# Performance work log

Hardware: AMD Instinct MI355X
Metric: run time of the kernel (lower is better)

## Reference

```python
import jax, jax.numpy as jnp
import numpy as np

N = 50000      # nodes
E = 800000     # edges (before self loops)
NFEAT = 128
HEADS = 4
NCLASS = 32    # per-head out channels of each GATConv
NHID = HEADS * NCLASS  # 128, inter-layer width
NEG_SLOPE = 0.2


def setup_inputs() -> dict:
    key = jax.random.key(0)
    ks = jax.random.split(key, 10)
    x = jax.random.normal(ks[0], (N, NFEAT), dtype=jnp.float32)
    adj = jax.random.randint(ks[1], (2, E), 0, N, dtype=jnp.int32)

    def glorot(k, shape):
        fan = shape[0] + shape[-1]
        return jax.random.normal(k, shape, dtype=jnp.float32) * jnp.sqrt(2.0 / fan)

    # conv1: nfeat -> heads*nclass
    W1 = glorot(ks[2], (NFEAT, HEADS * NCLASS))
    att_src1 = glorot(ks[3], (HEADS, NCLASS))
    att_dst1 = glorot(ks[4], (HEADS, NCLASS))
    b1 = jnp.zeros((HEADS * NCLASS,), dtype=jnp.float32)
    # conv2: nhid -> heads*nclass
    W2 = glorot(ks[5], (NHID, HEADS * NCLASS))
    att_src2 = glorot(ks[6], (HEADS, NCLASS))
    att_dst2 = glorot(ks[7], (HEADS, NCLASS))
    b2 = jnp.zeros((HEADS * NCLASS,), dtype=jnp.float32)
    return {"x": x, "adj": adj,
            "W1": W1, "att_src1": att_src1, "att_dst1": att_dst1, "b1": b1,
            "W2": W2, "att_src2": att_src2, "att_dst2": att_dst2, "b2": b2}


def gat_conv(x, src, dst, n, W, att_src, att_dst, bias):
    """PyG GATConv (concat=True, inference): gather -> edge attention -> segment softmax -> scatter."""
    H, C = att_src.shape
    h = (x @ W).reshape(n, H, C)                    # [N,H,C]
    a_s = jnp.sum(h * att_src[None], axis=-1)       # [N,H]
    a_d = jnp.sum(h * att_dst[None], axis=-1)       # [N,H]
    e = jax.nn.leaky_relu(a_s[src] + a_d[dst], NEG_SLOPE)  # [E,H]
    # numerically-stable segment softmax over edges grouped by destination node
    m = jax.ops.segment_max(e, dst, num_segments=n)        # [N,H]
    m = jnp.where(jnp.isfinite(m), m, 0.0)
    ex = jnp.exp(e - m[dst])                               # [E,H]
    denom = jax.ops.segment_sum(ex, dst, num_segments=n)   # [N,H]
    alpha = ex / (denom[dst] + 1e-16)                      # [E,H]
    out = jax.ops.segment_sum(h[src] * alpha[:, :, None], dst, num_segments=n)  # [N,H,C]
    return out.reshape(n, H * C) + bias


def reference(x, adj, W1, att_src1, att_dst1, b1, W2, att_src2, att_dst2, b2):
    # PyG GATConv adds self loops by default
    loops = jnp.arange(N, dtype=adj.dtype)
    src = jnp.concatenate([adj[0], loops])
    dst = jnp.concatenate([adj[1], loops])
    h = jax.nn.relu(gat_conv(x, src, dst, N, W1, att_src1, att_dst1, b1))
    # dropout is identity in eval mode
    out = gat_conv(h, src, dst, N, W2, att_src2, att_dst2, b2)
    return out
```

## Files before the change

### kernel.cpp

```cpp
#include <hip/hip_runtime.h>

#define N_NODES 50000
#define E_EDGES 800000
#define ETOT    (E_EDGES + N_NODES)
#define NF      128
#define HEADS   4
#define NC      32
#define LOG2E   1.44269504088896340736f
#define ASTRIDE 136
#define CAP     96

#define NBUCK   196
#define EPB     4096
#define NBLKA   ((ETOT + EPB - 1) / EPB)
#define PARTN   (NBUCK * NBLKA)
#define NBLKS   ((PARTN + 255) / 256)

typedef __attribute__((ext_vector_type(8))) short short8v;
typedef __attribute__((ext_vector_type(4))) float f32x4;

__device__ inline ushort rne_bf16(float x) {
    uint u = __float_as_uint(x);
    return (ushort)((u + 0x7fff + ((u >> 16) & 1)) >> 16);
}

__global__ __launch_bounds__(256) void pass_hist_kernel(const int* __restrict__ adj,
                                                        int* __restrict__ partials) {
    __shared__ int lc[NBUCK];
    int tid = threadIdx.x;
    for (int i = tid; i < NBUCK; i += 256) lc[i] = 0;
    __syncthreads();
    int base = blockIdx.x * EPB;
    #pragma unroll
    for (int i = 0; i < EPB / 256; ++i) {
        int e = base + i * 256 + tid;
        if (e < ETOT) {
            int dst = (e < E_EDGES) ? adj[E_EDGES + e] : (e - E_EDGES);
            atomicAdd(&lc[dst >> 8], 1);
        }
    }
    __syncthreads();
    for (int i = tid; i < NBUCK; i += 256) partials[i * NBLKA + blockIdx.x] = lc[i];
}

__device__ inline int block_incl_scan(int v, int* sh4) {
    int lane = threadIdx.x & 63, wid = threadIdx.x >> 6;
    int s = v;
    #pragma unroll
    for (int ofs = 1; ofs < 64; ofs <<= 1) {
        int t = __shfl_up(s, ofs);
        if (lane >= ofs) s += t;
    }
    if (lane == 63) sh4[wid] = s;
    __syncthreads();
    int add = 0;
    #pragma unroll
    for (int k = 0; k < 3; ++k) if (k < wid) add += sh4[k];
    return s + add;
}

__global__ __launch_bounds__(256) void bsum2_kernel(const int* __restrict__ partials,
                                                    int* __restrict__ bsum) {
    __shared__ int sh4[4];
    int i = blockIdx.x * 256 + threadIdx.x;
    int v = (i < PARTN) ? partials[i] : 0;
    int s = block_incl_scan(v, sh4);
    if (threadIdx.x == 255) bsum[blockIdx.x] = s;
}

__global__ __launch_bounds__(256) void scan_bsums2_kernel(const int* __restrict__ bsum,
                                                          int* __restrict__ bofs) {
    __shared__ int sh4[4];
    int i = threadIdx.x;
    int v = (i < NBLKS) ? bsum[i] : 0;
    int s = block_incl_scan(v, sh4);
    if (i < NBLKS) bofs[i] = s - v;
}

__global__ __launch_bounds__(256) void scan_final2_kernel(const int* __restrict__ partials,
                                                          const int* __restrict__ bofs,
                                                          int* __restrict__ pscan) {
    __shared__ int sh4[4];
    int i = blockIdx.x * 256 + threadIdx.x;
    int v = (i < PARTN) ? partials[i] : 0;
    int s = block_incl_scan(v, sh4);
    if (i < PARTN) pscan[i] = bofs[blockIdx.x] + s - v;
}

__global__ __launch_bounds__(256) void pass_scatter_kernel(const int* __restrict__ adj,
                                                           const int* __restrict__ pscan,
                                                           int2* __restrict__ ebuf) {
    __shared__ int lc[NBUCK];
    int tid = threadIdx.x;
    for (int i = tid; i < NBUCK; i += 256) lc[i] = 0;
    __syncthreads();
    int base = blockIdx.x * EPB;
    #pragma unroll
    for (int i = 0; i < EPB / 256; ++i) {
        int e = base + i * 256 + tid;
        if (e < ETOT) {
            int src, dst;
            if (e < E_EDGES) { src = adj[e]; dst = adj[E_EDGES + e]; }
            else             { src = dst = e - E_EDGES; }
            int b = dst >> 8;
            int r = atomicAdd(&lc[b], 1);
            int pos = pscan[b * NBLKA + blockIdx.x] + r;
            ebuf[pos] = make_int2(src, dst);
        }
    }
}

__global__ __launch_bounds__(256) void pass_build_kernel(const int2* __restrict__ ebuf,
                                                         const int* __restrict__ pscan,
                                                         int* __restrict__ cnt,
                                                         int* __restrict__ slots) {
    __shared__ int lc[256];
    int tid = threadIdx.x;
    int b = blockIdx.x;
    lc[tid] = 0;
    __syncthreads();
    int base = pscan[b * NBLKA];
    int end  = (b == NBUCK - 1) ? ETOT : pscan[(b + 1) * NBLKA];
    for (int e = base + tid; e < end; e += 256) {
        int2 sd = ebuf[e];
        int d = sd.y & 255;
        int r = atomicAdd(&lc[d], 1);
        slots[(size_t)sd.y * CAP + r] = sd.x;
    }
    __syncthreads();
    int dst = b * 256 + tid;
    if (dst < N_NODES) cnt[dst] = lc[tid];
}

__global__ __launch_bounds__(256) void wconv_kernel(const float* __restrict__ W,
                                                    const float* __restrict__ att_src,
                                                    const float* __restrict__ att_dst,
                                                    ushort* __restrict__ Wt) {
    int b = blockIdx.x, tid = threadIdx.x;
    if (b < 64) {
        int i = b * 256 + tid;
        int k = i >> 7, n = i & 127;
        Wt[n * 144 + k] = rne_bf16(W[i]);
    } else {
        for (int j = tid; j < 1024; j += 256) {
            int k = j >> 3, o = j & 7;
            int h = o & 3;
            const float* av = (o < 4) ? att_src : att_dst;
            float s = 0.f;
            #pragma unroll
            for (int c = 0; c < 32; ++c) s += W[k * 128 + h * 32 + c] * av[h * 32 + c];
            Wt[(128 + o) * 144 + k] = rne_bf16(s * LOG2E);
        }
        for (int j = tid; j < 8 * 144; j += 256)
            Wt[(136 + (j / 144)) * 144 + (j % 144)] = 0;
    }
}

__global__ __launch_bounds__(256) void gemm_mfma_kernel(const float* __restrict__ X,
                                                        const ushort* __restrict__ Wt,
                                                        ushort* __restrict__ Hbf,
                                                        float* __restrict__ a_s,
                                                        float* __restrict__ a_d, int nrows) {
    __shared__ ushort Abf[64 * ASTRIDE];
    int tid = threadIdx.x;
    int r0 = blockIdx.x * 64;

    {
        const float4* Xv = (const float4*)(X + (size_t)r0 * NF);
        int rleft = nrows - r0;
        #pragma unroll
        for (int p = 0; p < 8; ++p) {
            int i = p * 256 + tid;
            int row = i >> 5, c4 = i & 31;
            float4 v = (row < rleft) ? Xv[row * 32 + c4] : make_float4(0.f, 0.f, 0.f, 0.f);
            ushort4 hv;
            hv.x = rne_bf16(v.x); hv.y = rne_bf16(v.y);
            hv.z = rne_bf16(v.z); hv.w = rne_bf16(v.w);
            *(ushort4*)&Abf[row * ASTRIDE + c4 * 4] = hv;
        }
    }
    __syncthreads();

    int wv = tid >> 6;
    int l = tid & 63;
    int lr = l & 15;
    int lk = l >> 4;
    int rowb = wv * 16;

    short8v a[4];
    #pragma unroll
    for (int kc = 0; kc < 4; ++kc)
        a[kc] = *(const short8v*)&Abf[(rowb + lr) * ASTRIDE + kc * 32 + lk * 8];

    f32x4 acc[9];
    #pragma unroll
    for (int ct = 0; ct < 9; ++ct) acc[ct] = (f32x4){0.f, 0.f, 0.f, 0.f};

    #pragma unroll
    for (int ct = 0; ct < 9; ++ct) {
        #pragma unroll
        for (int kc = 0; kc < 4; ++kc) {
            short8v b = *(const short8v*)&Wt[(ct * 16 + lr) * 144 + kc * 32 + lk * 8];
            acc[ct] = __builtin_amdgcn_mfma_f32_16x16x32_bf16(a[kc], b, acc[ct], 0, 0, 0);
        }
    }

    int rbase = r0 + rowb + lk * 4;
    #pragma unroll
    for (int ct = 0; ct < 8; ++ct) {
        int col = ct * 16 + lr;
        #pragma unroll
        for (int ri = 0; ri < 4; ++ri) {
            int r = rbase + ri;
            if (r < nrows) Hbf[(size_t)r * NF + col] = rne_bf16(acc[ct][ri]);
        }
    }
    if (lr < 8) {
        #pragma unroll
        for (int ri = 0; ri < 4; ++ri) {
            int r = rbase + ri;
            if (r < nrows) {
                if (lr < 4) a_s[(size_t)r * 4 + lr] = acc[8][ri];
                else        a_d[(size_t)r * 4 + (lr - 4)] = acc[8][ri];
            }
        }
    }
}

__global__ __launch_bounds__(256) void agg_kernel(const ushort* __restrict__ Hbf,
                                                  const float* __restrict__ a_s,
                                                  const float* __restrict__ a_d,
                                                  const int* __restrict__ cnt,
                                                  const int* __restrict__ slots,
                                                  const float* __restrict__ bias,
                                                  float* __restrict__ Out, int relu) {
    int lane = threadIdx.x & 63;
    int node = blockIdx.x * 4 + (threadIdx.x >> 6);
    if (node >= N_NODES) return;
    int q = lane >> 4;
    int t = lane & 15;
    int h = t >> 2;
    float adn = a_d[node * 4 + h];
    int deg = cnt[node];
    const int* row = slots + node * CAP;
    const uint4* H4 = (const uint4*)Hbf;
    float acc[8];
    #pragma unroll
    for (int k = 0; k < 8; ++k) acc[k] = 0.f;
    float denom = 0.f;

    for (int j = 0; j < deg; j += 16) {
        int sv[4]; float ev[4]; uint4 hv[4]; bool ok[4];
        #pragma unroll
        for (int u = 0; u < 4; ++u) {
            int idx = j + u * 4 + q;
            ok[u] = idx < deg;
            sv[u] = row[ok[u] ? idx : 0];
        }
        #pragma unroll
        for (int u = 0; u < 4; ++u) ev[u] = a_s[sv[u] * 4 + h];
        #pragma unroll
        for (int u = 0; u < 4; ++u) hv[u] = H4[(size_t)sv[u] * 16 + t];
        #pragma unroll
        for (int u = 0; u < 4; ++u) {
            float e = ev[u] + adn;
            e = (e > 0.f) ? e : 0.2f * e;
            float w = ok[u] ? exp2f(e) : 0.f;
            denom += w;
            acc[0] += __uint_as_float(hv[u].x << 16) * w;
            acc[1] += __uint_as_float(hv[u].x & 0xffff0000u) * w;
            acc[2] += __uint_as_float(hv[u].y << 16) * w;
            acc[3] += __uint_as_float(hv[u].y & 0xffff0000u) * w;
            acc[4] += __uint_as_float(hv[u].z << 16) * w;
            acc[5] += __uint_as_float(hv[u].z & 0xffff0000u) * w;
            acc[6] += __uint_as_float(hv[u].w << 16) * w;
            acc[7] += __uint_as_float(hv[u].w & 0xffff0000u) * w;
        }
    }
    #pragma unroll
    for (int ofs = 16; ofs < 64; ofs <<= 1) {
        denom += __shfl_xor(denom, ofs);
        #pragma unroll
        for (int k = 0; k < 8; ++k) acc[k] += __shfl_xor(acc[k], ofs);
    }
    if (q == 0) {
        float inv = 1.f / (denom + 1e-16f);
        float4 b0 = ((const float4*)bias)[t * 2];
        float4 b1 = ((const float4*)bias)[t * 2 + 1];
        float4 o0 = make_float4(acc[0] * inv + b0.x, acc[1] * inv + b0.y,
                                acc[2] * inv + b0.z, acc[3] * inv + b0.w);
        float4 o1 = make_float4(acc[4] * inv + b1.x, acc[5] * inv + b1.y,
                                acc[6] * inv + b1.z, acc[7] * inv + b1.w);
        if (relu) {
            o0.x = fmaxf(o0.x, 0.f); o0.y = fmaxf(o0.y, 0.f);
            o0.z = fmaxf(o0.z, 0.f); o0.w = fmaxf(o0.w, 0.f);
            o1.x = fmaxf(o1.x, 0.f); o1.y = fmaxf(o1.y, 0.f);
            o1.z = fmaxf(o1.z, 0.f); o1.w = fmaxf(o1.w, 0.f);
        }
        float4* orow = (float4*)(Out + (size_t)node * NF);
        orow[t * 2]     = o0;
        orow[t * 2 + 1] = o1;
    }
}

extern "C" void kernel_launch(void* const* d_in, const int* in_sizes, int n_in,
                              void* d_out, int out_size, void* d_ws, size_t ws_size,
                              hipStream_t stream) {
    const float* x        = (const float*)d_in[0];
    const int*   adj      = (const int*)  d_in[1];
    const float* W1       = (const float*)d_in[2];
    const float* att_src1 = (const float*)d_in[3];
    const float* att_dst1 = (const float*)d_in[4];
    const float* b1       = (const float*)d_in[5];
    const float* W2       = (const float*)d_in[6];
    const float* att_src2 = (const float*)d_in[7];
    const float* att_dst2 = (const float*)d_in[8];
    const float* b2       = (const float*)d_in[9];
    float* out = (float*)d_out;

    float* obuf = (float*)d_ws;
    float* a_s  = obuf + (size_t)N_NODES * NF;
    float* a_d  = a_s + (size_t)N_NODES * HEADS;
    ushort* Hbf = (ushort*)(a_d + (size_t)N_NODES * HEADS);
    ushort* Wt  = Hbf + (size_t)N_NODES * NF;
    int* cnt     = (int*)(Wt + 144 * 144);
    int* slots   = cnt + N_NODES;
    int* partials= slots + (size_t)N_NODES * CAP;
    int* pscan   = partials + PARTN;
    int* bsum    = pscan + PARTN;
    int* bofs    = bsum + NBLKS;
    int2* ebuf   = (int2*)(bofs + NBLKS + 2);

    pass_hist_kernel<<<NBLKA, 256, 0, stream>>>(adj, partials);
    bsum2_kernel<<<NBLKS, 256, 0, stream>>>(partials, bsum);
    scan_bsums2_kernel<<<1, 256, 0, stream>>>(bsum, bofs);
    scan_final2_kernel<<<NBLKS, 256, 0, stream>>>(partials, bofs, pscan);
    pass_scatter_kernel<<<NBLKA, 256, 0, stream>>>(adj, pscan, ebuf);
    pass_build_kernel<<<NBUCK, 256, 0, stream>>>(ebuf, pscan, cnt, slots);

    wconv_kernel<<<65, 256, 0, stream>>>(W1, att_src1, att_dst1, Wt);
    gemm_mfma_kernel<<<(N_NODES + 63) / 64, 256, 0, stream>>>(x, Wt, Hbf, a_s, a_d, N_NODES);
    agg_kernel<<<(N_NODES + 3) / 4, 256, 0, stream>>>(Hbf, a_s, a_d, cnt, slots, b1, obuf, 1);

    wconv_kernel<<<65, 256, 0, stream>>>(W2, att_src2, att_dst2, Wt);
    gemm_mfma_kernel<<<(N_NODES + 63) / 64, 256, 0, stream>>>(obuf, Wt, Hbf, a_s, a_d, N_NODES);
    agg_kernel<<<(N_NODES + 3) / 4, 256, 0, stream>>>(Hbf, a_s, a_d, cnt, slots, b2, out, 0);
}
```

Baseline: 161.8 us.

## Fuse graph-build and weight prep kernels, single-pass lookback scan, fp16 features

Cuts the launch chain from 12 kernels to 7. The histogram is merged with both layers' weight conversions into one prep kernel. The three-kernel scan becomes a single-pass decoupled-lookback scan. Edge scattering shares a launch with the layer-1 GEMM. Intermediate features are stored as fp16 instead of bf16 and widened with half-to-float conversion in aggregation. This removes launch gaps and serial dependencies but adds spin-waiting in the scan, which assumes earlier tiles make forward progress, and changes the precision and range of the stored features.

```diff
diff --git a/kernel.cpp b/kernel.cpp
--- a/kernel.cpp
+++ b/kernel.cpp
@@ -1,4 +1,5 @@
 #include <hip/hip_runtime.h>
+#include <hip/hip_fp16.h>
 
 #define N_NODES 50000
 #define E_EDGES 800000
@@ -14,7 +15,8 @@
 #define EPB     4096
 #define NBLKA   ((ETOT + EPB - 1) / EPB)
 #define PARTN   (NBUCK * NBLKA)
-#define NBLKS   ((PARTN + 255) / 256)
+#define NTILES  ((PARTN + 255) / 256)
+#define WCB     65
 
 typedef __attribute__((ext_vector_type(8))) short short8v;
 typedef __attribute__((ext_vector_type(4))) float f32x4;
@@ -23,122 +25,15 @@
     uint u = __float_as_uint(x);
     return (ushort)((u + 0x7fff + ((u >> 16) & 1)) >> 16);
 }
-
-__global__ __launch_bounds__(256) void pass_hist_kernel(const int* __restrict__ adj,
-                                                        int* __restrict__ partials) {
-    __shared__ int lc[NBUCK];
-    int tid = threadIdx.x;
-    for (int i = tid; i < NBUCK; i += 256) lc[i] = 0;
-    __syncthreads();
-    int base = blockIdx.x * EPB;
-    #pragma unroll
-    for (int i = 0; i < EPB / 256; ++i) {
-        int e = base + i * 256 + tid;
-        if (e < ETOT) {
-            int dst = (e < E_EDGES) ? adj[E_EDGES + e] : (e - E_EDGES);
-            atomicAdd(&lc[dst >> 8], 1);
-        }
-    }
-    __syncthreads();
-    for (int i = tid; i < NBUCK; i += 256) partials[i * NBLKA + blockIdx.x] = lc[i];
-}
-
-__device__ inline int block_incl_scan(int v, int* sh4) {
-    int lane = threadIdx.x & 63, wid = threadIdx.x >> 6;
-    int s = v;
-    #pragma unroll
-    for (int ofs = 1; ofs < 64; ofs <<= 1) {
-        int t = __shfl_up(s, ofs);
-        if (lane >= ofs) s += t;
-    }
-    if (lane == 63) sh4[wid] = s;
-    __syncthreads();
-    int add = 0;
-    #pragma unroll
-    for (int k = 0; k < 3; ++k) if (k < wid) add += sh4[k];
-    return s + add;
-}
-
-__global__ __launch_bounds__(256) void bsum2_kernel(const int* __restrict__ partials,
-                                                    int* __restrict__ bsum) {
-    __shared__ int sh4[4];
-    int i = blockIdx.x * 256 + threadIdx.x;
-    int v = (i < PARTN) ? partials[i] : 0;
-    int s = block_incl_scan(v, sh4);
-    if (threadIdx.x == 255) bsum[blockIdx.x] = s;
-}
-
-__global__ __launch_bounds__(256) void scan_bsums2_kernel(const int* __restrict__ bsum,
-                                                          int* __restrict__ bofs) {
-    __shared__ int sh4[4];
-    int i = threadIdx.x;
-    int v = (i < NBLKS) ? bsum[i] : 0;
-    int s = block_incl_scan(v, sh4);
-    if (i < NBLKS) bofs[i] = s - v;
-}
-
-__global__ __launch_bounds__(256) void scan_final2_kernel(const int* __restrict__ partials,
-                                                          const int* __restrict__ bofs,
-                                                          int* __restrict__ pscan) {
-    __shared__ int sh4[4];
-    int i = blockIdx.x * 256 + threadIdx.x;
-    int v = (i < PARTN) ? partials[i] : 0;
-    int s = block_incl_scan(v, sh4);
-    if (i < PARTN) pscan[i] = bofs[blockIdx.x] + s - v;
-}
-
-__global__ __launch_bounds__(256) void pass_scatter_kernel(const int* __restrict__ adj,
-                                                           const int* __restrict__ pscan,
-                                                           int2* __restrict__ ebuf) {
-    __shared__ int lc[NBUCK];
-    int tid = threadIdx.x;
-    for (int i = tid; i < NBUCK; i += 256) lc[i] = 0;
-    __syncthreads();
-    int base = blockIdx.x * EPB;
-    #pragma unroll
-    for (int i = 0; i < EPB / 256; ++i) {
-        int e = base + i * 256 + tid;
-        if (e < ETOT) {
-            int src, dst;
-            if (e < E_EDGES) { src = adj[e]; dst = adj[E_EDGES + e]; }
-            else             { src = dst = e - E_EDGES; }
-            int b = dst >> 8;
-            int r = atomicAdd(&lc[b], 1);
-            int pos = pscan[b * NBLKA + blockIdx.x] + r;
-            ebuf[pos] = make_int2(src, dst);
-        }
-    }
-}
-
-__global__ __launch_bounds__(256) void pass_build_kernel(const int2* __restrict__ ebuf,
-                                                         const int* __restrict__ pscan,
-                                                         int* __restrict__ cnt,
-                                                         int* __restrict__ slots) {
-    __shared__ int lc[256];
-    int tid = threadIdx.x;
-    int b = blockIdx.x;
-    lc[tid] = 0;
-    __syncthreads();
-    int base = pscan[b * NBLKA];
-    int end  = (b == NBUCK - 1) ? ETOT : pscan[(b + 1) * NBLKA];
-    for (int e = base + tid; e < end; e += 256) {
-        int2 sd = ebuf[e];
-        int d = sd.y & 255;
-        int r = atomicAdd(&lc[d], 1);
-        slots[(size_t)sd.y * CAP + r] = sd.x;
-    }
-    __syncthreads();
-    int dst = b * 256 + tid;
-    if (dst < N_NODES) cnt[dst] = lc[tid];
-}
-
-__global__ __launch_bounds__(256) void wconv_kernel(const float* __restrict__ W,
-                                                    const float* __restrict__ att_src,
-                                                    const float* __restrict__ att_dst,
-                                                    ushort* __restrict__ Wt) {
-    int b = blockIdx.x, tid = threadIdx.x;
-    if (b < 64) {
-        int i = b * 256 + tid;
+__device__ inline float h2f_lo(uint u) { return __half2float(__ushort_as_half((ushort)(u & 0xffffu))); }
+__device__ inline float h2f_hi(uint u) { return __half2float(__ushort_as_half((ushort)(u >> 16))); }
+
+__device__ inline void wconv_body(int wb, int tid, const float* __restrict__ W,
+                                  const float* __restrict__ att_src,
+                                  const float* __restrict__ att_dst,
+                                  ushort* __restrict__ Wt) {
+    if (wb < 64) {
+        int i = wb * 256 + tid;
         int k = i >> 7, n = i & 127;
         Wt[n * 144 + k] = rne_bf16(W[i]);
     } else {
@@ -156,15 +51,99 @@
     }
 }
 
-__global__ __launch_bounds__(256) void gemm_mfma_kernel(const float* __restrict__ X,
-                                                        const ushort* __restrict__ Wt,
-                                                        ushort* __restrict__ Hbf,
-                                                        float* __restrict__ a_s,
-                                                        float* __restrict__ a_d, int nrows) {
-    __shared__ ushort Abf[64 * ASTRIDE];
-    int tid = threadIdx.x;
-    int r0 = blockIdx.x * 64;
-
+__global__ __launch_bounds__(256) void prep_kernel(const int* __restrict__ adj,
+                                                   int* __restrict__ partials,
+                                                   const float* __restrict__ W1,
+                                                   const float* __restrict__ as1,
+                                                   const float* __restrict__ ad1,
+                                                   ushort* __restrict__ Wt1,
+                                                   const float* __restrict__ W2,
+                                                   const float* __restrict__ as2,
+                                                   const float* __restrict__ ad2,
+                                                   ushort* __restrict__ Wt2,
+                                                   unsigned long long* __restrict__ tstate) {
+    __shared__ int lc[NBUCK];
+    int b = blockIdx.x, tid = threadIdx.x;
+    if (b < NBLKA) {
+        for (int i = tid; i < NBUCK; i += 256) lc[i] = 0;
+        __syncthreads();
+        int base = b * EPB;
+        #pragma unroll
+        for (int i = 0; i < EPB / 256; ++i) {
+            int e = base + i * 256 + tid;
+            if (e < ETOT) {
+                int dst = (e < E_EDGES) ? adj[E_EDGES + e] : (e - E_EDGES);
+                atomicAdd(&lc[dst >> 8], 1);
+            }
+        }
+        __syncthreads();
+        for (int i = tid; i < NBUCK; i += 256) partials[i * NBLKA + b] = lc[i];
+    } else {
+        if (b == NBLKA && tid < NTILES) tstate[tid] = 0ull;
+        int wb = b - NBLKA;
+        if (wb < WCB) wconv_body(wb, tid, W1, as1, ad1, Wt1);
+        else          wconv_body(wb - WCB, tid, W2, as2, ad2, Wt2);
+    }
+}
+
+__device__ inline int block_incl_scan(int v, int* sh4) {
+    int lane = threadIdx.x & 63, wid = threadIdx.x >> 6;
+    int s = v;
+    #pragma unroll
+    for (int ofs = 1; ofs < 64; ofs <<= 1) {
+        int t = __shfl_up(s, ofs);
+        if (lane >= ofs) s += t;
+    }
+    if (lane == 63) sh4[wid] = s;
+    __syncthreads();
+    int add = 0;
+    #pragma unroll
+    for (int k = 0; k < 3; ++k) if (k < wid) add += sh4[k];
+    return s + add;
+}
+
+__global__ __launch_bounds__(256) void scan_lookback_kernel(const int* __restrict__ partials,
+                                                            unsigned long long* __restrict__ tstate,
+                                                            int* __restrict__ pscan) {
+    __shared__ int sh4[4];
+    __shared__ int btot_sh, prefix_sh;
+    int tile = blockIdx.x, tid = threadIdx.x;
+    int i = tile * 256 + tid;
+    int v = (i < PARTN) ? partials[i] : 0;
+    int s = block_incl_scan(v, sh4);
+    if (tid == 255) btot_sh = s;
+    __syncthreads();
+    int btot = btot_sh;
+    if (tid == 0) {
+        if (tile == 0) {
+            __hip_atomic_store(&tstate[0], (2ull << 32) | (unsigned)btot,
+                               __ATOMIC_RELEASE, __HIP_MEMORY_SCOPE_AGENT);
+            prefix_sh = 0;
+        } else {
+            __hip_atomic_store(&tstate[tile], (1ull << 32) | (unsigned)btot,
+                               __ATOMIC_RELEASE, __HIP_MEMORY_SCOPE_AGENT);
+            int pfx = 0;
+            for (int p = tile - 1; p >= 0; --p) {
+                unsigned long long st;
+                do {
+                    st = __hip_atomic_load(&tstate[p], __ATOMIC_ACQUIRE, __HIP_MEMORY_SCOPE_AGENT);
+                } while ((st >> 32) == 0);
+                pfx += (int)(st & 0xffffffffu);
+                if ((st >> 32) == 2) break;
+            }
+            __hip_atomic_store(&tstate[tile], (2ull << 32) | (unsigned)(pfx + btot),
+                               __ATOMIC_RELEASE, __HIP_MEMORY_SCOPE_AGENT);
+            prefix_sh = pfx;
+        }
+    }
+    __syncthreads();
+    if (i < PARTN) pscan[i] = prefix_sh + s - v;
+}
+
+__device__ inline void gemm_body(ushort* __restrict__ Abf, int tid, int r0,
+                                 const float* __restrict__ X, const ushort* __restrict__ Wt,
+                                 ushort* __restrict__ Hf, float* __restrict__ a_s,
+                                 float* __restrict__ a_d, int nrows) {
     {
         const float4* Xv = (const float4*)(X + (size_t)r0 * NF);
         int rleft = nrows - r0;
@@ -212,7 +191,7 @@
         #pragma unroll
         for (int ri = 0; ri < 4; ++ri) {
             int r = rbase + ri;
-            if (r < nrows) Hbf[(size_t)r * NF + col] = rne_bf16(acc[ct][ri]);
+            if (r < nrows) Hf[(size_t)r * NF + col] = __half_as_ushort(__float2half(acc[ct][ri]));
         }
     }
     if (lr < 8) {
@@ -227,7 +206,70 @@
     }
 }
 
-__global__ __launch_bounds__(256) void agg_kernel(const ushort* __restrict__ Hbf,
+__global__ __launch_bounds__(256) void mid_kernel(const int* __restrict__ adj,
+                                                  const int* __restrict__ pscan,
+                                                  int2* __restrict__ ebuf,
+                                                  const float* __restrict__ X,
+                                                  const ushort* __restrict__ Wt,
+                                                  ushort* __restrict__ Hf,
+                                                  float* __restrict__ a_s,
+                                                  float* __restrict__ a_d, int nrows) {
+    __shared__ ushort Abf[64 * ASTRIDE];
+    __shared__ int lc[NBUCK];
+    int b = blockIdx.x, tid = threadIdx.x;
+    if (b < NBLKA) {
+        for (int i = tid; i < NBUCK; i += 256) lc[i] = 0;
+        __syncthreads();
+        int base = b * EPB;
+        #pragma unroll
+        for (int i = 0; i < EPB / 256; ++i) {
+            int e = base + i * 256 + tid;
+            if (e < ETOT) {
+                int src, dst;
+                if (e < E_EDGES) { src = adj[e]; dst = adj[E_EDGES + e]; }
+                else             { src = dst = e - E_EDGES; }
+                int bk = dst >> 8;
+                int r = atomicAdd(&lc[bk], 1);
+                ebuf[pscan[bk * NBLKA + b] + r] = make_int2(src, dst);
+            }
+        }
+    } else {
+        gemm_body(Abf, tid, (b - NBLKA) * 64, X, Wt, Hf, a_s, a_d, nrows);
+    }
+}
+
+__global__ __launch_bounds__(256) void gemm_mfma_kernel(const float* __restrict__ X,
+                                                        const ushort* __restrict__ Wt,
+                                                        ushort* __restrict__ Hf,
+                                                        float* __restrict__ a_s,
+                                                        float* __restrict__ a_d, int nrows) {
+    __shared__ ushort Abf[64 * ASTRIDE];
+    gemm_body(Abf, threadIdx.x, blockIdx.x * 64, X, Wt, Hf, a_s, a_d, nrows);
+}
+
+__global__ __launch_bounds__(256) void pass_build_kernel(const int2* __restrict__ ebuf,
+                                                         const int* __restrict__ pscan,
+                                                         int* __restrict__ cnt,
+                                                         int* __restrict__ slots) {
+    __shared__ int lc[256];
+    int tid = threadIdx.x;
+    int b = blockIdx.x;
+    lc[tid] = 0;
+    __syncthreads();
+    int base = pscan[b * NBLKA];
+    int end  = (b == NBUCK - 1) ? ETOT : pscan[(b + 1) * NBLKA];
+    for (int e = base + tid; e < end; e += 256) {
+        int2 sd = ebuf[e];
+        int d = sd.y & 255;
+        int r = atomicAdd(&lc[d], 1);
+        slots[(size_t)sd.y * CAP + r] = sd.x;
+    }
+    __syncthreads();
+    int dst = b * 256 + tid;
+    if (dst < N_NODES) cnt[dst] = lc[tid];
+}
+
+__global__ __launch_bounds__(256) void agg_kernel(const ushort* __restrict__ Hf,
                                                   const float* __restrict__ a_s,
                                                   const float* __restrict__ a_d,
                                                   const int* __restrict__ cnt,
@@ -242,8 +284,8 @@
     int h = t >> 2;
     float adn = a_d[node * 4 + h];
     int deg = cnt[node];
-    const int* row = slots + node * CAP;
-    const uint4* H4 = (const uint4*)Hbf;
+    const int* row = slots + (size_t)node * CAP;
+    const uint4* H4 = (const uint4*)Hf;
     float acc[8];
     #pragma unroll
     for (int k = 0; k < 8; ++k) acc[k] = 0.f;
@@ -267,14 +309,14 @@
             e = (e > 0.f) ? e : 0.2f * e;
             float w = ok[u] ? exp2f(e) : 0.f;
             denom += w;
-            acc[0] += __uint_as_float(hv[u].x << 16) * w;
-            acc[1] += __uint_as_float(hv[u].x & 0xffff0000u) * w;
-            acc[2] += __uint_as_float(hv[u].y << 16) * w;
-            acc[3] += __uint_as_float(hv[u].y & 0xffff0000u) * w;
-            acc[4] += __uint_as_float(hv[u].z << 16) * w;
-            acc[5] += __uint_as_float(hv[u].z & 0xffff0000u) * w;
-            acc[6] += __uint_as_float(hv[u].w << 16) * w;
-            acc[7] += __uint_as_float(hv[u].w & 0xffff0000u) * w;
+            acc[0] = fmaf(h2f_lo(hv[u].x), w, acc[0]);
+            acc[1] = fmaf(h2f_hi(hv[u].x), w, acc[1]);
+            acc[2] = fmaf(h2f_lo(hv[u].y), w, acc[2]);
+            acc[3] = fmaf(h2f_hi(hv[u].y), w, acc[3]);
+            acc[4] = fmaf(h2f_lo(hv[u].z), w, acc[4]);
+            acc[5] = fmaf(h2f_hi(hv[u].z), w, acc[5]);
+            acc[6] = fmaf(h2f_lo(hv[u].w), w, acc[6]);
+            acc[7] = fmaf(h2f_hi(hv[u].w), w, acc[7]);
         }
     }
     #pragma unroll
@@ -321,28 +363,24 @@
     float* obuf = (float*)d_ws;
     float* a_s  = obuf + (size_t)N_NODES * NF;
     float* a_d  = a_s + (size_t)N_NODES * HEADS;
-    ushort* Hbf = (ushort*)(a_d + (size_t)N_NODES * HEADS);
-    ushort* Wt  = Hbf + (size_t)N_NODES * NF;
-    int* cnt     = (int*)(Wt + 144 * 144);
-    int* slots   = cnt + N_NODES;
-    int* partials= slots + (size_t)N_NODES * CAP;
-    int* pscan   = partials + PARTN;
-    int* bsum    = pscan + PARTN;
-    int* bofs    = bsum + NBLKS;
-    int2* ebuf   = (int2*)(bofs + NBLKS + 2);
-
-    pass_hist_kernel<<<NBLKA, 256, 0, stream>>>(adj, partials);
-    bsum2_kernel<<<NBLKS, 256, 0, stream>>>(partials, bsum);
-    scan_bsums2_kernel<<<1, 256, 0, stream>>>(bsum, bofs);
-    scan_final2_kernel<<<NBLKS, 256, 0, stream>>>(partials, bofs, pscan);
-    pass_scatter_kernel<<<NBLKA, 256, 0, stream>>>(adj, pscan, ebuf);
+    ushort* Hf  = (ushort*)(a_d + (size_t)N_NODES * HEADS);
+    ushort* Wt1 = Hf + (size_t)N_NODES * NF;
+    ushort* Wt2 = Wt1 + 144 * 144;
+    int* cnt      = (int*)(Wt2 + 144 * 144);
+    int* partials = cnt + N_NODES;
+    int* pscan    = partials + PARTN;
+    unsigned long long* tstate = (unsigned long long*)(pscan + PARTN);
+    int2* ebuf  = (int2*)(tstate + NTILES);
+    int* slots  = (int*)(ebuf + ETOT);
+
+    prep_kernel<<<NBLKA + 2 * WCB, 256, 0, stream>>>(adj, partials,
+                                                     W1, att_src1, att_dst1, Wt1,
+                                                     W2, att_src2, att_dst2, Wt2, tstate);
+    scan_lookback_kernel<<<NTILES, 256, 0, stream>>>(partials, tstate, pscan);
+    mid_kernel<<<NBLKA + (N_NODES + 63) / 64, 256, 0, stream>>>(adj, pscan, ebuf,
+                                                                x, Wt1, Hf, a_s, a_d, N_NODES);
     pass_build_kernel<<<NBUCK, 256, 0, stream>>>(ebuf, pscan, cnt, slots);
-
-    wconv_kernel<<<65, 256, 0, stream>>>(W1, att_src1, att_dst1, Wt);
-    gemm_mfma_kernel<<<(N_NODES + 63) / 64, 256, 0, stream>>>(x, Wt, Hbf, a_s, a_d, N_NODES);
-    agg_kernel<<<(N_NODES + 3) / 4, 256, 0, stream>>>(Hbf, a_s, a_d, cnt, slots, b1, obuf, 1);
-
-    wconv_kernel<<<65, 256, 0, stream>>>(W2, att_src2, att_dst2, Wt);
-    gemm_mfma_kernel<<<(N_NODES + 63) / 64, 256, 0, stream>>>(obuf, Wt, Hbf, a_s, a_d, N_NODES);
-    agg_kernel<<<(N_NODES + 3) / 4, 256, 0, stream>>>(Hbf, a_s, a_d, cnt, slots, b2, out, 0);
-}
+    agg_kernel<<<(N_NODES + 3) / 4, 256, 0, stream>>>(Hf, a_s, a_d, cnt, slots, b1, obuf, 1);
+    gemm_mfma_kernel<<<(N_NODES + 63) / 64, 256, 0, stream>>>(obuf, Wt2, Hf, a_s, a_d, N_NODES);
+    agg_kernel<<<(N_NODES + 3) / 4, 256, 0, stream>>>(Hf, a_s, a_d, cnt, slots, b2, out, 0);
+}
```

Measured after the change: 172.0 us. +6.3%, slower.
